# Optimization experiments

Measured on AMD Instinct MI355X. Metric: run time of the kernel, lower is better.

## Reference

```python
import jax, jax.numpy as jnp
import numpy as np

NUM_HEADS = 16


def setup_inputs() -> dict:
    key = jax.random.key(0)
    k1, k2, k3 = jax.random.split(key, 3)
    B, N, D = 4, 1024, 1024
    x = jax.random.normal(k1, (B, N, D), dtype=jnp.float32)
    w_qkv = jax.random.normal(k2, (3 * D, D), dtype=jnp.float32) * (D ** -0.5)
    w_out = jax.random.normal(k3, (D, D), dtype=jnp.float32) * (D ** -0.5)
    b_out = jnp.zeros((D,), dtype=jnp.float32)
    return {"x": x, "w_qkv": w_qkv, "w_out": w_out, "b_out": b_out}


def reference(x, w_qkv, w_out, b_out):
    B, N, D = x.shape
    H = NUM_HEADS
    d = D // H
    scale = d ** -0.5
    # qkv projection (no bias): [B,N,3D] -> [B,N,3,H,d]
    qkv = jnp.einsum('bnd,ed->bne', x, w_qkv).reshape(B, N, 3, H, d)
    # -> [3, B, H, N, d]
    qkv = jnp.transpose(qkv, (2, 0, 3, 1, 4))
    q, k, v = qkv[0], qkv[1], qkv[2]
    # attention scores [B,H,N,N], stable softmax
    scores = jnp.einsum('bhqd,bhkd->bhqk', q, k) * scale
    attn = jax.nn.softmax(scores, axis=-1)
    out = jnp.einsum('bhqk,bhkd->bhqd', attn, v)  # [B,H,N,d]
    out = jnp.transpose(out, (0, 2, 1, 3)).reshape(B, N, D)
    # output projection with bias
    return jnp.einsum('bnd,ed->bne', out, w_out) + b_out
```

## Files before the change

kernel.cpp:

```cpp
#include <hip/hip_runtime.h>
#include <stdint.h>

typedef __bf16 bf16_t;
typedef bf16_t bf16x8 __attribute__((ext_vector_type(8)));
typedef float f32x4 __attribute__((ext_vector_type(4)));

static __device__ __forceinline__ unsigned short f2bf(float f) {
    union { float f; unsigned int u; } v; v.f = f;
    unsigned int u = v.u;
    unsigned int r = (u + 0x7fffu + ((u >> 16) & 1u)) >> 16;
    return (unsigned short)r;
}

static __device__ __forceinline__ bf16x8 as_frag(uint4 v) {
    union { uint4 u; bf16x8 b; } c; c.u = v; return c.b;
}

static __device__ __forceinline__ unsigned int fbits(float f) {
    union { float f; unsigned int u; } v; v.f = f; return v.u;
}
static __device__ __forceinline__ float fval(unsigned int u) {
    union { unsigned int u; float f; } v; v.u = u; return v.f;
}

static __device__ __forceinline__ void gl2lds16(const unsigned short* g, uint4* l) {
    __builtin_amdgcn_global_load_lds(
        (const __attribute__((address_space(1))) unsigned int*)g,
        (__attribute__((address_space(3))) unsigned int*)l, 16, 0, 0);
}

#define MFMA16(a, b, c) __builtin_amdgcn_mfma_f32_16x16x32_bf16((a), (b), (c), 0, 0, 0)

#define QSCALE 0.1803368801111204f

__global__ void cvt_all(const float* __restrict__ x,
                        const float* __restrict__ wq,
                        const float* __restrict__ wo,
                        unsigned short* __restrict__ xb,
                        unsigned short* __restrict__ wqb,
                        unsigned short* __restrict__ wob) {
    const float* in; unsigned short* out; int n4;
    if (blockIdx.y == 0)      { in = x;  out = xb;  n4 = 1048576; }
    else if (blockIdx.y == 1) { in = wq; out = wqb; n4 = 786432; }
    else                      { in = wo; out = wob; n4 = 262144; }
    for (int i = blockIdx.x * 256 + threadIdx.x; i < n4; i += 1024 * 256) {
        float4 v = ((const float4*)in)[i];
        ushort4 o;
        o.x = f2bf(v.x); o.y = f2bf(v.y); o.z = f2bf(v.z); o.w = f2bf(v.w);
        ((ushort4*)out)[i] = o;
    }
}

template <int OUTMODE>
__global__ __launch_bounds__(256, 2) void gemm_bt(
    const unsigned short* __restrict__ A,
    const unsigned short* __restrict__ B,
    void* __restrict__ Cv,
    const float* __restrict__ bias,
    unsigned short* __restrict__ Vt,
    int M, int N, int K) {
    __shared__ uint4 As[1024];
    __shared__ uint4 Bs[1024];
    const int tid  = threadIdx.x;
    const int lane = tid & 63;
    const int wave = tid >> 6;
    const int quad = lane >> 4;
    const int l16  = lane & 15;
    const int wr   = (wave >> 1) * 64;
    const int wc   = (wave & 1) * 64;
    const int bm   = blockIdx.y * 128;
    const int bn   = blockIdx.x * 128;

    f32x4 zero4 = {0.f, 0.f, 0.f, 0.f};
    f32x4 acc[4][4];
#pragma unroll
    for (int mt = 0; mt < 4; ++mt)
#pragma unroll
        for (int nt = 0; nt < 4; ++nt) acc[mt][nt] = zero4;

    const int s_row = tid >> 3;
    const int s_kcs = tid & 7;

    for (int k0 = 0; k0 < K; k0 += 64) {
        __syncthreads();
#pragma unroll
        for (int i = 0; i < 4; ++i) {
            int s   = i * 256 + tid;
            int row = i * 32 + s_row;
            int kcg = s_kcs ^ (row & 7);
            gl2lds16(A + (size_t)(bm + row) * K + k0 + kcg * 8, &As[s]);
            gl2lds16(B + (size_t)(bn + row) * K + k0 + kcg * 8, &Bs[s]);
        }
        __syncthreads();
#pragma unroll
        for (int ks = 0; ks < 2; ++ks) {
            int kc = ks * 4 + quad;
            bf16x8 af[4], bff[4];
#pragma unroll
            for (int mt = 0; mt < 4; ++mt) {
                int row = wr + mt * 16 + l16;
                af[mt] = as_frag(As[row * 8 + (kc ^ (row & 7))]);
            }
#pragma unroll
            for (int nt = 0; nt < 4; ++nt) {
                int row = wc + nt * 16 + l16;
                bff[nt] = as_frag(Bs[row * 8 + (kc ^ (row & 7))]);
            }
#pragma unroll
            for (int mt = 0; mt < 4; ++mt)
#pragma unroll
                for (int nt = 0; nt < 4; ++nt)
                    acc[mt][nt] = MFMA16(af[mt], bff[nt], acc[mt][nt]);
        }
    }

    if (OUTMODE == 1) {
        float* C = (float*)Cv;
#pragma unroll
        for (int mt = 0; mt < 4; ++mt)
#pragma unroll
            for (int nt = 0; nt < 4; ++nt) {
                int col = bn + wc + nt * 16 + l16;
                float bv = bias ? bias[col] : 0.f;
#pragma unroll
                for (int r = 0; r < 4; ++r) {
                    int row = bm + wr + mt * 16 + quad * 4 + r;
                    C[(size_t)row * N + col] = acc[mt][nt][r] + bv;
                }
            }
    } else if (OUTMODE == 0) {
        unsigned short* C = (unsigned short*)Cv;
#pragma unroll
        for (int mt = 0; mt < 4; ++mt)
#pragma unroll
            for (int nt = 0; nt < 4; ++nt) {
                int col = bn + wc + nt * 16 + l16;
#pragma unroll
                for (int r = 0; r < 4; ++r) {
                    int row = bm + wr + mt * 16 + quad * 4 + r;
                    C[(size_t)row * N + col] = f2bf(acc[mt][nt][r]);
                }
            }
    } else {
        if (bn < 2048) {
            unsigned short* C = (unsigned short*)Cv;
#pragma unroll
            for (int mt = 0; mt < 4; ++mt)
#pragma unroll
                for (int nt = 0; nt < 4; ++nt) {
                    int col = bn + wc + nt * 16 + l16;
                    float sc = (col < 1024) ? QSCALE : 1.0f;
#pragma unroll
                    for (int r = 0; r < 4; ++r) {
                        int row = bm + wr + mt * 16 + quad * 4 + r;
                        C[(size_t)row * 2048 + col] = f2bf(acc[mt][nt][r] * sc);
                    }
                }
        } else {
#pragma unroll
            for (int mt = 0; mt < 4; ++mt)
#pragma unroll
                for (int nt = 0; nt < 4; ++nt) {
                    int col = bn + wc + nt * 16 + l16 - 2048;
                    int h = col >> 6, dd = col & 63;
                    int token0 = bm + wr + mt * 16 + quad * 4;
                    int b = token0 >> 10, t = token0 & 1023;
                    ushort4 pk;
                    pk.x = f2bf(acc[mt][nt][0]);
                    pk.y = f2bf(acc[mt][nt][1]);
                    pk.z = f2bf(acc[mt][nt][2]);
                    pk.w = f2bf(acc[mt][nt][3]);
                    *(ushort4*)(Vt + ((size_t)((b * 16 + h) * 64 + dd) * 1024 + t)) = pk;
                }
        }
    }
}

__global__ __launch_bounds__(256, 2) void attn_kernel(
    const unsigned short* __restrict__ qk,
    const unsigned short* __restrict__ vt,
    unsigned short* __restrict__ out) {
    __shared__ uint4 Ps[1024];
    __shared__ uint4 Ks[2][1024];
    __shared__ uint4 Vs[2][1024];

    const int tid  = threadIdx.x;
    const int lane = tid & 63;
    const int wave = tid >> 6;
    const int quad = lane >> 4;
    const int l16  = lane & 15;
    const int bh   = blockIdx.x;
    const int b    = bh >> 4, h = bh & 15;
    const int qbase = blockIdx.y * 128;
    const size_t rowbase = (size_t)b * 1024;
    const int hoff = h * 64;

    const int st_row = tid >> 3;
    const int st_kcs = tid & 7;
    const int sv_dd  = tid >> 4;
    const int sv_tcs = tid & 15;
    const unsigned short* kp0 = qk + rowbase * 2048 + 1024 + hoff;
    const unsigned short* vp0 = vt + (size_t)bh * 65536;

#pragma unroll
    for (int p = 0; p < 4; ++p) {
        int row = p * 32 + st_row;
        int kcg = st_kcs ^ (row & 7);
        gl2lds16(kp0 + (size_t)row * 2048 + kcg * 8, &Ks[0][p * 256 + tid]);
        gl2lds16(qk + (rowbase + qbase + row) * 2048 + hoff + kcg * 8,
                 &Ps[p * 256 + tid]);
        int dd = p * 16 + sv_dd;
        int tcg = sv_tcs ^ (dd & 7);
        gl2lds16(vp0 + (size_t)dd * 1024 + tcg * 8, &Vs[0][p * 256 + tid]);
    }
    __syncthreads();

    bf16x8 qf[2][2];
#pragma unroll
    for (int sub = 0; sub < 2; ++sub)
#pragma unroll
        for (int ks = 0; ks < 2; ++ks) {
            int kc = ks * 4 + quad;
            int row = wave * 32 + sub * 16 + l16;
            qf[sub][ks] = as_frag(Ps[row * 8 + (kc ^ (row & 7))]);
        }

    f32x4 zero4 = {0.f, 0.f, 0.f, 0.f};
    f32x4 Oacc[2][4];
#pragma unroll
    for (int sub = 0; sub < 2; ++sub)
#pragma unroll
        for (int no = 0; no < 4; ++no) Oacc[sub][no] = zero4;
    float lsum[2] = {0.f, 0.f};

    uint4* const Pw = Ps + wave * 256;

    for (int kt = 0; kt < 8; ++kt) {
        const int buf = kt & 1;
        if (kt) __syncthreads();
        if (kt < 7) {
#pragma unroll
            for (int p = 0; p < 4; ++p) {
                int row = p * 32 + st_row;
                int kcg = st_kcs ^ (row & 7);
                gl2lds16(kp0 + (size_t)((kt + 1) * 128 + row) * 2048 + kcg * 8,
                         &Ks[buf ^ 1][p * 256 + tid]);
                int dd = p * 16 + sv_dd;
                int tcg = sv_tcs ^ (dd & 7);
                gl2lds16(vp0 + (size_t)dd * 1024 + (kt + 1) * 128 + tcg * 8,
                         &Vs[buf ^ 1][p * 256 + tid]);
            }
        }

        f32x4 st[2][8];
#pragma unroll
        for (int sub = 0; sub < 2; ++sub)
#pragma unroll
            for (int nt = 0; nt < 8; ++nt) st[sub][nt] = zero4;
#pragma unroll
        for (int ks = 0; ks < 2; ++ks) {
            int kc = ks * 4 + quad;
#pragma unroll
            for (int nt = 0; nt < 8; ++nt) {
                int row = nt * 16 + l16;
                bf16x8 kf = as_frag(Ks[buf][row * 8 + (kc ^ (row & 7))]);
                st[0][nt] = MFMA16(kf, qf[0][ks], st[0][nt]);
                st[1][nt] = MFMA16(kf, qf[1][ks], st[1][nt]);
            }
        }

        unsigned int pw[2][8][2];
#pragma unroll
        for (int sub = 0; sub < 2; ++sub) {
            float rs = 0.f;
#pragma unroll
            for (int nt = 0; nt < 8; ++nt) {
                unsigned int b0 = fbits(__builtin_amdgcn_exp2f(st[sub][nt][0])) & 0xffff0000u;
                unsigned int b1 = fbits(__builtin_amdgcn_exp2f(st[sub][nt][1])) & 0xffff0000u;
                unsigned int b2 = fbits(__builtin_amdgcn_exp2f(st[sub][nt][2])) & 0xffff0000u;
                unsigned int b3 = fbits(__builtin_amdgcn_exp2f(st[sub][nt][3])) & 0xffff0000u;
                rs += (fval(b0) + fval(b1)) + (fval(b2) + fval(b3));
                pw[sub][nt][0] = __builtin_amdgcn_perm(b1, b0, 0x07060302u);
                pw[sub][nt][1] = __builtin_amdgcn_perm(b3, b2, 0x07060302u);
            }
            lsum[sub] += rs;
        }

#pragma unroll
        for (int hf = 0; hf < 2; ++hf) {
#pragma unroll
            for (int sub = 0; sub < 2; ++sub) {
                int row = sub * 16 + l16;
#pragma unroll
                for (int t = 0; t < 4; ++t) {
                    int kc = t * 2 + (quad >> 1);
                    uint2 w2 = make_uint2(pw[sub][hf * 4 + t][0], pw[sub][hf * 4 + t][1]);
                    ((uint2*)Pw)[(row * 8 + (kc ^ (row & 7))) * 2 + (quad & 1)] = w2;
                }
            }
#pragma unroll
            for (int k2 = 0; k2 < 2; ++k2) {
                int kc = k2 * 4 + quad;
                bf16x8 pf[2];
#pragma unroll
                for (int sub = 0; sub < 2; ++sub) {
                    int row = sub * 16 + l16;
                    pf[sub] = as_frag(Pw[row * 8 + (kc ^ (row & 7))]);
                }
                int tc = (hf * 2 + k2) * 4 + quad;
#pragma unroll
                for (int no = 0; no < 4; ++no) {
                    int dd = no * 16 + l16;
                    bf16x8 vf = as_frag(Vs[buf][dd * 16 + (tc ^ (dd & 7))]);
                    Oacc[0][no] = MFMA16(pf[0], vf, Oacc[0][no]);
                    Oacc[1][no] = MFMA16(pf[1], vf, Oacc[1][no]);
                }
            }
        }
    }

#pragma unroll
    for (int sub = 0; sub < 2; ++sub) {
        lsum[sub] += __shfl_xor(lsum[sub], 16, 64);
        lsum[sub] += __shfl_xor(lsum[sub], 32, 64);
        float linv = 1.f / lsum[sub];
#pragma unroll
        for (int r = 0; r < 4; ++r) {
            float iv = __shfl(linv, quad * 4 + r, 64);
            int qrow = qbase + wave * 32 + sub * 16 + quad * 4 + r;
#pragma unroll
            for (int no = 0; no < 4; ++no) {
                int dd = no * 16 + l16;
                out[(rowbase + qrow) * 1024 + hoff + dd] = f2bf(Oacc[sub][no][r] * iv);
            }
        }
    }
}

extern "C" void kernel_launch(void* const* d_in, const int* in_sizes, int n_in,
                              void* d_out, int out_size, void* d_ws, size_t ws_size,
                              hipStream_t stream) {
    const float* x     = (const float*)d_in[0];
    const float* w_qkv = (const float*)d_in[1];
    const float* w_out = (const float*)d_in[2];
    const float* b_out = (const float*)d_in[3];

    char* ws = (char*)d_ws;
    unsigned short* wqkvb = (unsigned short*)(ws);
    unsigned short* woutb = (unsigned short*)(ws + 6291456);
    unsigned short* qkb   = (unsigned short*)(ws + 8388608);
    unsigned short* vtb   = (unsigned short*)(ws + 25165824);
    unsigned short* xb    = (unsigned short*)(ws + 33554432);
    unsigned short* attnb = xb;

    cvt_all<<<dim3(1024, 3), 256, 0, stream>>>(x, w_qkv, w_out, xb, wqkvb, woutb);

    gemm_bt<2><<<dim3(24, 32), 256, 0, stream>>>(xb, wqkvb, (void*)qkb, nullptr,
                                                 vtb, 4096, 3072, 1024);
    attn_kernel<<<dim3(64, 8), 256, 0, stream>>>(qkb, vtb, attnb);
    gemm_bt<1><<<dim3(8, 32), 256, 0, stream>>>(attnb, woutb, d_out, b_out,
                                                nullptr, 4096, 1024, 1024);
}
```

Measured before the change: 167.0 us.

## Shrink attention KV tiles and output-projection GEMM tile to raise occupancy

The attention kernel now streams K/V in 64-token tiles instead of 128, which halves its shared-memory buffers and score registers, and it writes P to LDS straight after exponentiation. Launch bounds go from 2 to 3 blocks per CU for both kernels. The GEMM is templated on its M tile, and the output projection now uses 64-row tiles, doubling its grid to 512 blocks so more CUs have work. In exchange there are twice as many attention loop iterations and barriers, and less data reuse per block in the smaller GEMM tiles.

```diff
diff --git a/kernel.cpp b/kernel.cpp
--- a/kernel.cpp
+++ b/kernel.cpp
@@ -51,30 +51,31 @@
     }
 }
 
-template <int OUTMODE>
-__global__ __launch_bounds__(256, 2) void gemm_bt(
+template <int OUTMODE, int BM>
+__global__ __launch_bounds__(256, 3) void gemm_bt(
     const unsigned short* __restrict__ A,
     const unsigned short* __restrict__ B,
     void* __restrict__ Cv,
     const float* __restrict__ bias,
     unsigned short* __restrict__ Vt,
     int M, int N, int K) {
-    __shared__ uint4 As[1024];
+    constexpr int MT = BM / 32;
+    __shared__ uint4 As[BM * 8];
     __shared__ uint4 Bs[1024];
     const int tid  = threadIdx.x;
     const int lane = tid & 63;
     const int wave = tid >> 6;
     const int quad = lane >> 4;
     const int l16  = lane & 15;
-    const int wr   = (wave >> 1) * 64;
+    const int wr   = (wave >> 1) * (BM / 2);
     const int wc   = (wave & 1) * 64;
-    const int bm   = blockIdx.y * 128;
+    const int bm   = blockIdx.y * BM;
     const int bn   = blockIdx.x * 128;
 
     f32x4 zero4 = {0.f, 0.f, 0.f, 0.f};
-    f32x4 acc[4][4];
-#pragma unroll
-    for (int mt = 0; mt < 4; ++mt)
+    f32x4 acc[MT][4];
+#pragma unroll
+    for (int mt = 0; mt < MT; ++mt)
 #pragma unroll
         for (int nt = 0; nt < 4; ++nt) acc[mt][nt] = zero4;
 
@@ -84,20 +85,24 @@
     for (int k0 = 0; k0 < K; k0 += 64) {
         __syncthreads();
 #pragma unroll
-        for (int i = 0; i < 4; ++i) {
-            int s   = i * 256 + tid;
+        for (int i = 0; i < MT; ++i) {
             int row = i * 32 + s_row;
             int kcg = s_kcs ^ (row & 7);
-            gl2lds16(A + (size_t)(bm + row) * K + k0 + kcg * 8, &As[s]);
-            gl2lds16(B + (size_t)(bn + row) * K + k0 + kcg * 8, &Bs[s]);
+            gl2lds16(A + (size_t)(bm + row) * K + k0 + kcg * 8, &As[i * 256 + tid]);
+        }
+#pragma unroll
+        for (int i = 0; i < 4; ++i) {
+            int row = i * 32 + s_row;
+            int kcg = s_kcs ^ (row & 7);
+            gl2lds16(B + (size_t)(bn + row) * K + k0 + kcg * 8, &Bs[i * 256 + tid]);
         }
         __syncthreads();
 #pragma unroll
         for (int ks = 0; ks < 2; ++ks) {
             int kc = ks * 4 + quad;
-            bf16x8 af[4], bff[4];
-#pragma unroll
-            for (int mt = 0; mt < 4; ++mt) {
+            bf16x8 af[MT], bff[4];
+#pragma unroll
+            for (int mt = 0; mt < MT; ++mt) {
                 int row = wr + mt * 16 + l16;
                 af[mt] = as_frag(As[row * 8 + (kc ^ (row & 7))]);
             }
@@ -107,7 +112,7 @@
                 bff[nt] = as_frag(Bs[row * 8 + (kc ^ (row & 7))]);
             }
 #pragma unroll
-            for (int mt = 0; mt < 4; ++mt)
+            for (int mt = 0; mt < MT; ++mt)
 #pragma unroll
                 for (int nt = 0; nt < 4; ++nt)
                     acc[mt][nt] = MFMA16(af[mt], bff[nt], acc[mt][nt]);
@@ -117,7 +122,7 @@
     if (OUTMODE == 1) {
         float* C = (float*)Cv;
 #pragma unroll
-        for (int mt = 0; mt < 4; ++mt)
+        for (int mt = 0; mt < MT; ++mt)
 #pragma unroll
             for (int nt = 0; nt < 4; ++nt) {
                 int col = bn + wc + nt * 16 + l16;
@@ -131,7 +136,7 @@
     } else if (OUTMODE == 0) {
         unsigned short* C = (unsigned short*)Cv;
 #pragma unroll
-        for (int mt = 0; mt < 4; ++mt)
+        for (int mt = 0; mt < MT; ++mt)
 #pragma unroll
             for (int nt = 0; nt < 4; ++nt) {
                 int col = bn + wc + nt * 16 + l16;
@@ -145,7 +150,7 @@
         if (bn < 2048) {
             unsigned short* C = (unsigned short*)Cv;
 #pragma unroll
-            for (int mt = 0; mt < 4; ++mt)
+            for (int mt = 0; mt < MT; ++mt)
 #pragma unroll
                 for (int nt = 0; nt < 4; ++nt) {
                     int col = bn + wc + nt * 16 + l16;
@@ -158,7 +163,7 @@
                 }
         } else {
 #pragma unroll
-            for (int mt = 0; mt < 4; ++mt)
+            for (int mt = 0; mt < MT; ++mt)
 #pragma unroll
                 for (int nt = 0; nt < 4; ++nt) {
                     int col = bn + wc + nt * 16 + l16 - 2048;
@@ -176,13 +181,13 @@
     }
 }
 
-__global__ __launch_bounds__(256, 2) void attn_kernel(
+__global__ __launch_bounds__(256, 3) void attn_kernel(
     const unsigned short* __restrict__ qk,
     const unsigned short* __restrict__ vt,
     unsigned short* __restrict__ out) {
     __shared__ uint4 Ps[1024];
-    __shared__ uint4 Ks[2][1024];
-    __shared__ uint4 Vs[2][1024];
+    __shared__ uint4 Ks[2][512];
+    __shared__ uint4 Vs[2][512];
 
     const int tid  = threadIdx.x;
     const int lane = tid & 63;
@@ -196,22 +201,23 @@
     const int hoff = h * 64;
 
     const int st_row = tid >> 3;
-    const int st_kcs = tid & 7;
-    const int sv_dd  = tid >> 4;
-    const int sv_tcs = tid & 15;
+    const int st_c   = tid & 7;
     const unsigned short* kp0 = qk + rowbase * 2048 + 1024 + hoff;
     const unsigned short* vp0 = vt + (size_t)bh * 65536;
 
 #pragma unroll
+    for (int p = 0; p < 2; ++p) {
+        int row = p * 32 + st_row;
+        int cg = st_c ^ (row & 7);
+        gl2lds16(kp0 + (size_t)row * 2048 + cg * 8, &Ks[0][p * 256 + tid]);
+        gl2lds16(vp0 + (size_t)row * 1024 + cg * 8, &Vs[0][p * 256 + tid]);
+    }
+#pragma unroll
     for (int p = 0; p < 4; ++p) {
         int row = p * 32 + st_row;
-        int kcg = st_kcs ^ (row & 7);
-        gl2lds16(kp0 + (size_t)row * 2048 + kcg * 8, &Ks[0][p * 256 + tid]);
-        gl2lds16(qk + (rowbase + qbase + row) * 2048 + hoff + kcg * 8,
+        int cg = st_c ^ (row & 7);
+        gl2lds16(qk + (rowbase + qbase + row) * 2048 + hoff + cg * 8,
                  &Ps[p * 256 + tid]);
-        int dd = p * 16 + sv_dd;
-        int tcg = sv_tcs ^ (dd & 7);
-        gl2lds16(vp0 + (size_t)dd * 1024 + tcg * 8, &Vs[0][p * 256 + tid]);
     }
     __syncthreads();
 
@@ -235,33 +241,31 @@
 
     uint4* const Pw = Ps + wave * 256;
 
-    for (int kt = 0; kt < 8; ++kt) {
+    for (int kt = 0; kt < 16; ++kt) {
         const int buf = kt & 1;
         if (kt) __syncthreads();
-        if (kt < 7) {
-#pragma unroll
-            for (int p = 0; p < 4; ++p) {
+        if (kt < 15) {
+#pragma unroll
+            for (int p = 0; p < 2; ++p) {
                 int row = p * 32 + st_row;
-                int kcg = st_kcs ^ (row & 7);
-                gl2lds16(kp0 + (size_t)((kt + 1) * 128 + row) * 2048 + kcg * 8,
+                int cg = st_c ^ (row & 7);
+                gl2lds16(kp0 + (size_t)((kt + 1) * 64 + row) * 2048 + cg * 8,
                          &Ks[buf ^ 1][p * 256 + tid]);
-                int dd = p * 16 + sv_dd;
-                int tcg = sv_tcs ^ (dd & 7);
-                gl2lds16(vp0 + (size_t)dd * 1024 + (kt + 1) * 128 + tcg * 8,
+                gl2lds16(vp0 + (size_t)row * 1024 + (kt + 1) * 64 + cg * 8,
                          &Vs[buf ^ 1][p * 256 + tid]);
             }
         }
 
-        f32x4 st[2][8];
+        f32x4 st[2][4];
 #pragma unroll
         for (int sub = 0; sub < 2; ++sub)
 #pragma unroll
-            for (int nt = 0; nt < 8; ++nt) st[sub][nt] = zero4;
+            for (int nt = 0; nt < 4; ++nt) st[sub][nt] = zero4;
 #pragma unroll
         for (int ks = 0; ks < 2; ++ks) {
             int kc = ks * 4 + quad;
 #pragma unroll
-            for (int nt = 0; nt < 8; ++nt) {
+            for (int nt = 0; nt < 4; ++nt) {
                 int row = nt * 16 + l16;
                 bf16x8 kf = as_frag(Ks[buf][row * 8 + (kc ^ (row & 7))]);
                 st[0][nt] = MFMA16(kf, qf[0][ks], st[0][nt]);
@@ -269,52 +273,41 @@
             }
         }
 
-        unsigned int pw[2][8][2];
 #pragma unroll
         for (int sub = 0; sub < 2; ++sub) {
+            int row = sub * 16 + l16;
             float rs = 0.f;
 #pragma unroll
-            for (int nt = 0; nt < 8; ++nt) {
+            for (int nt = 0; nt < 4; ++nt) {
                 unsigned int b0 = fbits(__builtin_amdgcn_exp2f(st[sub][nt][0])) & 0xffff0000u;
                 unsigned int b1 = fbits(__builtin_amdgcn_exp2f(st[sub][nt][1])) & 0xffff0000u;
                 unsigned int b2 = fbits(__builtin_amdgcn_exp2f(st[sub][nt][2])) & 0xffff0000u;
                 unsigned int b3 = fbits(__builtin_amdgcn_exp2f(st[sub][nt][3])) & 0xffff0000u;
                 rs += (fval(b0) + fval(b1)) + (fval(b2) + fval(b3));
-                pw[sub][nt][0] = __builtin_amdgcn_perm(b1, b0, 0x07060302u);
-                pw[sub][nt][1] = __builtin_amdgcn_perm(b3, b2, 0x07060302u);
+                uint2 w2;
+                w2.x = __builtin_amdgcn_perm(b1, b0, 0x07060302u);
+                w2.y = __builtin_amdgcn_perm(b3, b2, 0x07060302u);
+                int kc = nt * 2 + (quad >> 1);
+                ((uint2*)Pw)[(row * 8 + (kc ^ (row & 7))) * 2 + (quad & 1)] = w2;
             }
             lsum[sub] += rs;
         }
 
 #pragma unroll
-        for (int hf = 0; hf < 2; ++hf) {
+        for (int k2 = 0; k2 < 2; ++k2) {
+            int kc = k2 * 4 + quad;
+            bf16x8 pf[2];
 #pragma unroll
             for (int sub = 0; sub < 2; ++sub) {
                 int row = sub * 16 + l16;
-#pragma unroll
-                for (int t = 0; t < 4; ++t) {
-                    int kc = t * 2 + (quad >> 1);
-                    uint2 w2 = make_uint2(pw[sub][hf * 4 + t][0], pw[sub][hf * 4 + t][1]);
-                    ((uint2*)Pw)[(row * 8 + (kc ^ (row & 7))) * 2 + (quad & 1)] = w2;
-                }
-            }
-#pragma unroll
-            for (int k2 = 0; k2 < 2; ++k2) {
-                int kc = k2 * 4 + quad;
-                bf16x8 pf[2];
-#pragma unroll
-                for (int sub = 0; sub < 2; ++sub) {
-                    int row = sub * 16 + l16;
-                    pf[sub] = as_frag(Pw[row * 8 + (kc ^ (row & 7))]);
-                }
-                int tc = (hf * 2 + k2) * 4 + quad;
-#pragma unroll
-                for (int no = 0; no < 4; ++no) {
-                    int dd = no * 16 + l16;
-                    bf16x8 vf = as_frag(Vs[buf][dd * 16 + (tc ^ (dd & 7))]);
-                    Oacc[0][no] = MFMA16(pf[0], vf, Oacc[0][no]);
-                    Oacc[1][no] = MFMA16(pf[1], vf, Oacc[1][no]);
-                }
+                pf[sub] = as_frag(Pw[row * 8 + (kc ^ (row & 7))]);
+            }
+#pragma unroll
+            for (int no = 0; no < 4; ++no) {
+                int dd = no * 16 + l16;
+                bf16x8 vf = as_frag(Vs[buf][dd * 8 + (kc ^ (dd & 7))]);
+                Oacc[0][no] = MFMA16(pf[0], vf, Oacc[0][no]);
+                Oacc[1][no] = MFMA16(pf[1], vf, Oacc[1][no]);
             }
         }
     }
@@ -355,9 +348,9 @@
 
     cvt_all<<<dim3(1024, 3), 256, 0, stream>>>(x, w_qkv, w_out, xb, wqkvb, woutb);
 
-    gemm_bt<2><<<dim3(24, 32), 256, 0, stream>>>(xb, wqkvb, (void*)qkb, nullptr,
-                                                 vtb, 4096, 3072, 1024);
+    gemm_bt<2, 128><<<dim3(24, 32), 256, 0, stream>>>(xb, wqkvb, (void*)qkb,
+                                                      nullptr, vtb, 4096, 3072, 1024);
     attn_kernel<<<dim3(64, 8), 256, 0, stream>>>(qkb, vtb, attnb);
-    gemm_bt<1><<<dim3(8, 32), 256, 0, stream>>>(attnb, woutb, d_out, b_out,
-                                                nullptr, 4096, 1024, 1024);
-}
+    gemm_bt<1, 64><<<dim3(8, 64), 256, 0, stream>>>(attnb, woutb, d_out, b_out,
+                                                    nullptr, 4096, 1024, 1024);
+}
```

After: 158.6 us. -5.1%, faster.
